# Optimization experiments

Hardware: AMD Instinct MI355X
Metric: run time of the kernel (lower is better)

## Reference

```python
import jax, jax.numpy as jnp
import numpy as np

B, N, K = 16, 2048, 20
EPS = 1e-5
NEG_SLOPE = 0.01


def gsa(x, k):
    # graph_self_attention. x: (B, D, N)
    xx = jnp.sum(x * x, axis=1)                              # (B, N)
    inner = jnp.einsum('bdn,bdm->bnm', x, x)                 # (B, N, N)
    dist = 2.0 * inner - xx[:, :, None] - xx[:, None, :]
    s, idx = jax.lax.top_k(dist, k)                          # (B, N, k) nearest (incl. self)
    xt = jnp.transpose(x, (0, 2, 1))                         # (B, N, D)
    nn_feat = jax.vmap(lambda f, i: f[i])(xt, idx)           # (B, N, k, D) irregular gather
    diff = nn_feat - xt[:, :, None, :]                       # neighbor - center
    w = jax.nn.softmax(s, axis=-1)                           # (B, N, k)
    agg = jnp.einsum('bnk,bnkd->bnd', w, diff)               # (B, N, D)
    return jnp.transpose(jnp.concatenate([xt, agg], axis=2), (0, 2, 1))  # (B, 2D, N)


def conv_bn_lrelu(x, W, gamma, beta):
    # 1x1 Conv1d (no bias) + BatchNorm1d (training-mode batch stats) + LeakyReLU(0.01)
    y = jnp.einsum('oc,bcn->bon', W, x)
    mean = jnp.mean(y, axis=(0, 2), keepdims=True)
    var = jnp.var(y, axis=(0, 2), keepdims=True)
    y = (y - mean) * jax.lax.rsqrt(var + EPS)
    y = gamma[None, :, None] * y + beta[None, :, None]
    return jnp.where(y >= 0, y, NEG_SLOPE * y)


def setup_inputs() -> dict:
    key = jax.random.key(0)
    ks = jax.random.split(key, 6)
    x = jax.random.normal(ks[0], (B, 3, N), jnp.float32)

    def w(kk, o, c):
        return jax.random.normal(kk, (o, c), jnp.float32) * (1.0 / np.sqrt(c).astype(np.float32))

    inp = {
        'x': x,
        'W1': w(ks[1], 64, 6),
        'W2': w(ks[2], 64, 128),
        'W3': w(ks[3], 128, 128),
        'W4': w(ks[4], 256, 256),
        'W5': w(ks[5], 512, 512),
    }
    for i, c in zip(range(1, 6), (64, 64, 128, 256, 512)):
        inp[f'g{i}'] = jnp.ones((c,), jnp.float32)
        inp[f'b{i}'] = jnp.zeros((c,), jnp.float32)
    return inp


def reference(x, W1, W2, W3, W4, W5, g1, b1, g2, b2, g3, b3, g4, b4, g5, b5):
    k = K
    x1 = conv_bn_lrelu(gsa(x, k), W1, g1, b1)     # (B, 64, N)
    x2 = conv_bn_lrelu(gsa(x1, k), W2, g2, b2)    # (B, 64, N)
    x3 = conv_bn_lrelu(gsa(x2, k), W3, g3, b3)    # (B, 128, N)
    x4 = conv_bn_lrelu(gsa(x3, k), W4, g4, b4)    # (B, 256, N)
    cat = jnp.concatenate([x1, x2, x3, x4], axis=1)  # (B, 512, N)
    x5 = conv_bn_lrelu(cat, W5, g5, b5)              # (B, 512, N)
    return (x5, x3)
```

## Files before the change

kernel.cpp:

```cpp
#include <hip/hip_runtime.h>
#include <math.h>

#define B_ 16
#define N_ 2048
#define KNN 20
#define BN_EPS 1e-5f
#define SLOPE 0.01f

__global__ __launch_bounds__(256) void xx_kernel(const float* __restrict__ xin, long bstr, int D,
                                                 float* __restrict__ xx) {
  int i = blockIdx.x * 256 + threadIdx.x;
  if (i >= B_ * N_) return;
  int b = i >> 11, n = i & (N_ - 1);
  const float* p = xin + (long)b * bstr + n;
  float s = 0.f;
#pragma unroll 1
  for (int d = 0; d < D; ++d) { float v = p[(long)d * N_]; s = fmaf(v, v, s); }
  xx[i] = s;
}

__global__ __launch_bounds__(256) void transpose_kernel(const float* __restrict__ xin, long bstr,
                                                        float* __restrict__ xT, long xTbstr, int D) {
  __shared__ float s[32][65];
  int b = blockIdx.y;
  int n0 = blockIdx.x * 64;
  int tid = threadIdx.x;
  const float* xb = xin + (long)b * bstr;
  float* tb = xT + (long)b * xTbstr;
  for (int dc = 0; dc < D; dc += 32) {
    for (int i = tid; i < 32 * 64; i += 256) {
      int d = i >> 6, n = i & 63;
      s[d][n] = (dc + d < D) ? xb[(long)(dc + d) * N_ + n0 + n] : 0.f;
    }
    __syncthreads();
    for (int i = tid; i < 64 * 32; i += 256) {
      int n = i >> 5, d = i & 31;
      if (dc + d < D) tb[(long)(n0 + n) * D + dc + d] = s[d][n];
    }
    __syncthreads();
  }
}

template <int D>
__global__ __launch_bounds__(256, 2) void gsa_stream_kernel(const float* __restrict__ xin, long bstr,
                                                            const float* __restrict__ xT, long xTbstr,
                                                            const float* __restrict__ xx,
                                                            float* __restrict__ agg, long aggbstr) {
  constexpr int NV = (D + 63) / 64;
  __shared__ float xn_s[16][((D + 3) & ~3)];
  int tid = threadIdx.x, w = tid >> 6, lane = tid & 63;
  int r0 = blockIdx.x * 16;
  int b = r0 >> 11, n0 = r0 & (N_ - 1);
  const float* xb = xin + (long)b * bstr;
  const float* tb = xT + (long)b * xTbstr;
  for (int i = tid; i < 16 * D; i += 256) {
    int rr = i / D, d = i - rr * D;
    xn_s[rr][d] = tb[(long)(n0 + rr) * D + d];
  }
  __syncthreads();

  float4 acc[4][8];
#pragma unroll
  for (int r = 0; r < 4; ++r)
#pragma unroll
    for (int c = 0; c < 8; ++c) acc[r][c] = make_float4(0.f, 0.f, 0.f, 0.f);

  float4 bufA[8], bufB[8];
  {
    const float4* xrow = (const float4*)xb;
#pragma unroll
    for (int c = 0; c < 8; ++c) bufA[c] = xrow[c * 64 + lane];
  }

#define FMA_STEP(BUF, dd)                                              \
  {                                                                    \
    _Pragma("unroll") for (int r = 0; r < 4; ++r) {                    \
      float xnd = xn_s[(w << 2) + r][dd];                              \
      _Pragma("unroll") for (int c = 0; c < 8; ++c) {                  \
        acc[r][c].x = fmaf(xnd, BUF[c].x, acc[r][c].x);                \
        acc[r][c].y = fmaf(xnd, BUF[c].y, acc[r][c].y);                \
        acc[r][c].z = fmaf(xnd, BUF[c].z, acc[r][c].z);                \
        acc[r][c].w = fmaf(xnd, BUF[c].w, acc[r][c].w);                \
      }                                                                \
    }                                                                  \
  }

#pragma unroll 1
  for (int d = 0; d < D; d += 2) {
    if (d + 1 < D) {
      const float4* xrow = (const float4*)(xb + (long)(d + 1) * N_);
#pragma unroll
      for (int c = 0; c < 8; ++c) bufB[c] = xrow[c * 64 + lane];
    }
    FMA_STEP(bufA, d);
    if (d + 2 < D) {
      const float4* xrow = (const float4*)(xb + (long)(d + 2) * N_);
#pragma unroll
      for (int c = 0; c < 8; ++c) bufA[c] = xrow[c * 64 + lane];
    }
    if (d + 1 < D) FMA_STEP(bufB, d + 1);
  }
#undef FMA_STEP

  {
    const float4* xx4 = (const float4*)(xx + (long)b * N_);
    float4 xm[8];
#pragma unroll
    for (int c = 0; c < 8; ++c) xm[c] = xx4[c * 64 + lane];
#pragma unroll
    for (int r = 0; r < 4; ++r) {
      float xxn = xx[(long)b * N_ + n0 + (w << 2) + r];
#pragma unroll
      for (int c = 0; c < 8; ++c) {
        acc[r][c].x = 2.f * acc[r][c].x - xxn - xm[c].x;
        acc[r][c].y = 2.f * acc[r][c].y - xxn - xm[c].y;
        acc[r][c].z = 2.f * acc[r][c].z - xxn - xm[c].z;
        acc[r][c].w = 2.f * acc[r][c].w - xxn - xm[c].w;
      }
    }
  }

  float m8[4][8];
  int sspack[4];
#pragma unroll
  for (int r = 0; r < 4; ++r) {
    int sp = 0;
#pragma unroll
    for (int c = 0; c < 8; ++c) {
      const float* av = (const float*)&acc[r][c];
      float mm = av[0]; int ss = 0;
      if (av[1] > mm) { mm = av[1]; ss = 1; }
      if (av[2] > mm) { mm = av[2]; ss = 2; }
      if (av[3] > mm) { mm = av[3]; ss = 3; }
      m8[r][c] = mm; sp |= ss << (2 * c);
    }
    sspack[r] = sp;
  }

  float Z[4] = {0.f, 0.f, 0.f, 0.f};
  float m0[4];
  float ve[4][NV];
#pragma unroll
  for (int r = 0; r < 4; ++r)
#pragma unroll
    for (int vi = 0; vi < NV; ++vi) ve[r][vi] = 0.f;

#pragma unroll 1
  for (int it = 0; it < KNN; ++it) {
    float best[4]; int bidx[4];
#pragma unroll
    for (int r = 0; r < 4; ++r) {
      int sp = sspack[r];
      float bv = m8[r][0]; int bi = (lane << 2) + (sp & 3);
#pragma unroll
      for (int c = 1; c < 8; ++c) {
        float v = m8[r][c];
        int cand = (c << 8) + (lane << 2) + ((sp >> (2 * c)) & 3);
        if (v > bv) { bv = v; bi = cand; }
      }
      best[r] = bv; bidx[r] = bi;
    }
#pragma unroll
    for (int off = 1; off < 64; off <<= 1) {
#pragma unroll
      for (int r = 0; r < 4; ++r) {
        float ov = __shfl_xor(best[r], off);
        int oi = __shfl_xor(bidx[r], off);
        if (ov > best[r] || (ov == best[r] && oi < bidx[r])) { best[r] = ov; bidx[r] = oi; }
      }
    }
#pragma unroll
    for (int r = 0; r < 4; ++r) {
      int ub = __builtin_amdgcn_readfirstlane(bidx[r]);
      if (it == 0) m0[r] = best[r];
      float e = __expf(best[r] - m0[r]);
      Z[r] += e;
#pragma unroll
      for (int vi = 0; vi < NV; ++vi) {
        int dd = lane + (vi << 6);
        if (D >= 64 || dd < D) ve[r][vi] = fmaf(e, tb[(long)ub * D + dd], ve[r][vi]);
      }
      int cw = ub >> 8, jw = ub & 3;
      bool isw = (lane == ((ub >> 2) & 63));
#pragma unroll
      for (int c = 0; c < 8; ++c)
        if (c == cw) {
          float* av = (float*)&acc[r][c];
#pragma unroll
          for (int j = 0; j < 4; ++j)
            if (j == jw && isw) av[j] = -3.4e38f;
          float mm = av[0]; int ss = 0;
          if (av[1] > mm) { mm = av[1]; ss = 1; }
          if (av[2] > mm) { mm = av[2]; ss = 2; }
          if (av[3] > mm) { mm = av[3]; ss = 3; }
          m8[r][c] = mm;
          sspack[r] = (sspack[r] & ~(3 << (2 * c))) | (ss << (2 * c));
        }
    }
  }

#pragma unroll
  for (int r = 0; r < 4; ++r) {
    float rZ = 1.f / Z[r];
    int n = n0 + (w << 2) + r;
#pragma unroll
    for (int vi = 0; vi < NV; ++vi) {
      int dd = lane + (vi << 6);
      if (D >= 64 || dd < D)
        agg[(long)b * aggbstr + (long)dd * N_ + n] = ve[r][vi] * rZ - xn_s[(w << 2) + r][dd];
    }
  }
}

__global__ __launch_bounds__(256) void gemm_bn_kernel(const float* __restrict__ Wm, int O, int K,
                                                      const float* __restrict__ xin, long bstr, int Dx,
                                                      const float* __restrict__ agg, long aggbstr,
                                                      float* __restrict__ y, float* __restrict__ stats) {
  __shared__ __align__(16) float As[16][68];
  __shared__ __align__(16) float Bs[16][68];
  int tid = threadIdx.x;
  int o0 = blockIdx.x * 64;
  int j0 = blockIdx.y * 64;
  int b = j0 >> 11, n0 = j0 & (N_ - 1);
  int ty = tid >> 4, tx = tid & 15;
  float accr[4][4] = {};
  int aK = tid & 15, aO = tid >> 4;
  int bK = tid >> 4, bn4 = (tid & 15) << 2;
  for (int k0 = 0; k0 < K; k0 += 16) {
#pragma unroll
    for (int q = 0; q < 4; ++q) {
      int o = aO + (q << 4);
      As[aK][o] = (k0 + aK < K) ? Wm[(long)(o0 + o) * K + k0 + aK] : 0.f;
    }
    {
      int c = k0 + bK;
      float4 v = {0.f, 0.f, 0.f, 0.f};
      if (c < K) {
        const float* src = (c < Dx) ? xin + (long)b * bstr + (long)c * N_
                                    : agg + (long)b * aggbstr + (long)(c - Dx) * N_;
        v = *(const float4*)(src + n0 + bn4);
      }
      *(float4*)&Bs[bK][bn4] = v;
    }
    __syncthreads();
#pragma unroll
    for (int kk = 0; kk < 16; ++kk) {
      float4 a4 = *(const float4*)&As[kk][ty << 2];
      float4 b4 = *(const float4*)&Bs[kk][tx << 2];
      accr[0][0] = fmaf(a4.x, b4.x, accr[0][0]);
      accr[0][1] = fmaf(a4.x, b4.y, accr[0][1]);
      accr[0][2] = fmaf(a4.x, b4.z, accr[0][2]);
      accr[0][3] = fmaf(a4.x, b4.w, accr[0][3]);
      accr[1][0] = fmaf(a4.y, b4.x, accr[1][0]);
      accr[1][1] = fmaf(a4.y, b4.y, accr[1][1]);
      accr[1][2] = fmaf(a4.y, b4.z, accr[1][2]);
      accr[1][3] = fmaf(a4.y, b4.w, accr[1][3]);
      accr[2][0] = fmaf(a4.z, b4.x, accr[2][0]);
      accr[2][1] = fmaf(a4.z, b4.y, accr[2][1]);
      accr[2][2] = fmaf(a4.z, b4.z, accr[2][2]);
      accr[2][3] = fmaf(a4.z, b4.w, accr[2][3]);
      accr[3][0] = fmaf(a4.w, b4.x, accr[3][0]);
      accr[3][1] = fmaf(a4.w, b4.y, accr[3][1]);
      accr[3][2] = fmaf(a4.w, b4.z, accr[3][2]);
      accr[3][3] = fmaf(a4.w, b4.w, accr[3][3]);
    }
    __syncthreads();
  }
#pragma unroll
  for (int r = 0; r < 4; ++r) {
    int o = o0 + (ty << 2) + r;
    float4 v;
    v.x = accr[r][0]; v.y = accr[r][1]; v.z = accr[r][2]; v.w = accr[r][3];
    *(float4*)(y + ((long)b * O + o) * N_ + n0 + bn4) = v;
    float s1 = v.x + v.y + v.z + v.w;
    float s2 = v.x * v.x + v.y * v.y + v.z * v.z + v.w * v.w;
#pragma unroll
    for (int off = 1; off < 16; off <<= 1) { s1 += __shfl_xor(s1, off); s2 += __shfl_xor(s2, off); }
    if (tx == 0) { atomicAdd(&stats[o], s1); atomicAdd(&stats[O + o], s2); }
  }
}

__global__ __launch_bounds__(256) void gemm_bn128_kernel(const float* __restrict__ Wm, int O, int K,
                                                         const float* __restrict__ xin, long bstr, int Dx,
                                                         const float* __restrict__ agg, long aggbstr,
                                                         float* __restrict__ y, float* __restrict__ stats) {
  __shared__ __align__(16) float As[8][132];
  __shared__ __align__(16) float Bs[8][132];
  int tid = threadIdx.x;
  int o0 = blockIdx.x * 128;
  int j0 = blockIdx.y * 128;
  int b = j0 >> 11, n0 = j0 & (N_ - 1);
  int ty = tid >> 4, tx = tid & 15;
  float acc[8][8] = {};
  int aO = tid & 127, aKb = tid >> 7;
  int bK = tid >> 5, bj4 = (tid & 31) << 2;
#pragma unroll 1
  for (int k0 = 0; k0 < K; k0 += 8) {
    __syncthreads();
#pragma unroll
    for (int q = 0; q < 4; ++q) {
      int kk = aKb + (q << 1);
      As[kk][aO] = Wm[(long)(o0 + aO) * K + k0 + kk];
    }
    {
      int c = k0 + bK;
      const float* src = (c < Dx) ? xin + (long)b * bstr + (long)c * N_
                                  : agg + (long)b * aggbstr + (long)(c - Dx) * N_;
      *(float4*)&Bs[bK][bj4] = *(const float4*)(src + n0 + bj4);
    }
    __syncthreads();
#pragma unroll
    for (int kk = 0; kk < 8; ++kk) {
      float4 alo = *(const float4*)&As[kk][ty << 2];
      float4 ahi = *(const float4*)&As[kk][64 + (ty << 2)];
      float4 blo = *(const float4*)&Bs[kk][tx << 2];
      float4 bhi = *(const float4*)&Bs[kk][64 + (tx << 2)];
      float av[8] = {alo.x, alo.y, alo.z, alo.w, ahi.x, ahi.y, ahi.z, ahi.w};
      float bv[8] = {blo.x, blo.y, blo.z, blo.w, bhi.x, bhi.y, bhi.z, bhi.w};
#pragma unroll
      for (int r = 0; r < 8; ++r)
#pragma unroll
        for (int c = 0; c < 8; ++c) acc[r][c] = fmaf(av[r], bv[c], acc[r][c]);
    }
  }
#pragma unroll
  for (int r = 0; r < 8; ++r) {
    int o = o0 + ((r < 4) ? (ty << 2) + r : 64 + (ty << 2) + (r - 4));
    float4 vlo, vhi;
    vlo.x = acc[r][0]; vlo.y = acc[r][1]; vlo.z = acc[r][2]; vlo.w = acc[r][3];
    vhi.x = acc[r][4]; vhi.y = acc[r][5]; vhi.z = acc[r][6]; vhi.w = acc[r][7];
    float* yrow = y + ((long)b * O + o) * N_ + n0;
    *(float4*)(yrow + (tx << 2)) = vlo;
    *(float4*)(yrow + 64 + (tx << 2)) = vhi;
    float s1 = vlo.x + vlo.y + vlo.z + vlo.w + vhi.x + vhi.y + vhi.z + vhi.w;
    float s2 = vlo.x * vlo.x + vlo.y * vlo.y + vlo.z * vlo.z + vlo.w * vlo.w +
               vhi.x * vhi.x + vhi.y * vhi.y + vhi.z * vhi.z + vhi.w * vhi.w;
#pragma unroll
    for (int off = 1; off < 16; off <<= 1) { s1 += __shfl_xor(s1, off); s2 += __shfl_xor(s2, off); }
    if (tx == 0) { atomicAdd(&stats[o], s1); atomicAdd(&stats[O + o], s2); }
  }
}

__global__ __launch_bounds__(256) void bn_finalize_kernel(float* __restrict__ stats,
                                                          const float* __restrict__ g,
                                                          const float* __restrict__ be, int O) {
  int o = blockIdx.x * 256 + threadIdx.x;
  if (o >= O) return;
  const float inv_cnt = 1.f / (B_ * (float)N_);
  float mean = stats[o] * inv_cnt;
  float var = stats[O + o] * inv_cnt - mean * mean;
  float a = g[o] * rsqrtf(var + BN_EPS);
  float bb = be[o] - mean * a;
  stats[o] = a;
  stats[O + o] = bb;
}

__global__ __launch_bounds__(256) void bn_apply_kernel(const float* __restrict__ y,
                                                       const float* __restrict__ stats, int O,
                                                       float* __restrict__ dst, int c0, int dstStride,
                                                       float* __restrict__ dst2) {
  long i4 = (long)blockIdx.x * 256 + threadIdx.x;
  long total4 = (long)B_ * O * N_ / 4;
  if (i4 >= total4) return;
  long i = i4 << 2;
  int ob = __ffs(O) - 1;
  int o = (int)((i >> 11) & (O - 1));
  int b = (int)(i >> (11 + ob));
  int n = (int)(i & (N_ - 1));
  float a = stats[o], bb = stats[O + o];
  float4 v = *(const float4*)(y + i);
  v.x = fmaf(a, v.x, bb); v.x = v.x >= 0.f ? v.x : SLOPE * v.x;
  v.y = fmaf(a, v.y, bb); v.y = v.y >= 0.f ? v.y : SLOPE * v.y;
  v.z = fmaf(a, v.z, bb); v.z = v.z >= 0.f ? v.z : SLOPE * v.z;
  v.w = fmaf(a, v.w, bb); v.w = v.w >= 0.f ? v.w : SLOPE * v.w;
  *(float4*)(dst + ((long)b * dstStride + c0 + o) * N_ + n) = v;
  if (dst2) *(float4*)(dst2 + i) = v;
}

extern "C" void kernel_launch(void* const* d_in, const int* in_sizes, int n_in,
                              void* d_out, int out_size, void* d_ws, size_t ws_size,
                              hipStream_t stream) {
  const float* x = (const float*)d_in[0];
  const float* W[5];
  const float* gm[5];
  const float* bt[5];
  for (int i = 0; i < 5; ++i) W[i] = (const float*)d_in[1 + i];
  for (int i = 0; i < 5; ++i) { gm[i] = (const float*)d_in[6 + 2 * i]; bt[i] = (const float*)d_in[7 + 2 * i]; }

  const long XBS = 512L * N_;
  float* xall = (float*)d_ws;
  float* xxb = xall + (long)B_ * XBS;
  float* stats = xxb + (long)B_ * N_;
  float* xTb = xall + 256L * N_;
  float* aggb = xall + 384L * N_;
  float* yb = (float*)d_out;
  float* outB = (float*)d_out + (long)B_ * XBS;

  hipMemsetAsync(stats, 0, 5 * 1024 * sizeof(float), stream);

  struct LayerCfg { const float* xin; long bstr; int D; int O; int c0; };
  LayerCfg L[4] = {
      {x, 3L * N_, 3, 64, 0},
      {xall, XBS, 64, 64, 64},
      {xall + 64L * N_, XBS, 64, 128, 128},
      {xall + 128L * N_, XBS, 128, 256, 256},
  };

  for (int li = 0; li < 4; ++li) {
    const LayerCfg c = L[li];
    float* st = stats + li * 1024;
    xx_kernel<<<B_ * N_ / 256, 256, 0, stream>>>(c.xin, c.bstr, c.D, xxb);
    transpose_kernel<<<dim3(N_ / 64, B_), 256, 0, stream>>>(c.xin, c.bstr, xTb, XBS, c.D);
    if (c.D == 3)
      gsa_stream_kernel<3><<<B_ * N_ / 16, 256, 0, stream>>>(c.xin, c.bstr, xTb, XBS, xxb, aggb, XBS);
    else if (c.D == 64)
      gsa_stream_kernel<64><<<B_ * N_ / 16, 256, 0, stream>>>(c.xin, c.bstr, xTb, XBS, xxb, aggb, XBS);
    else
      gsa_stream_kernel<128><<<B_ * N_ / 16, 256, 0, stream>>>(c.xin, c.bstr, xTb, XBS, xxb, aggb, XBS);
    int K = 2 * c.D;
    if (c.O >= 128 && (K % 8) == 0)
      gemm_bn128_kernel<<<dim3(c.O / 128, B_ * N_ / 128), 256, 0, stream>>>(
          W[li], c.O, K, c.xin, c.bstr, c.D, aggb, XBS, yb, st);
    else
      gemm_bn_kernel<<<dim3(c.O / 64, B_ * N_ / 64), 256, 0, stream>>>(
          W[li], c.O, K, c.xin, c.bstr, c.D, aggb, XBS, yb, st);
    bn_finalize_kernel<<<(c.O + 255) / 256, 256, 0, stream>>>(st, gm[li], bt[li], c.O);
    long t4 = (long)B_ * c.O * N_ / 4;
    bn_apply_kernel<<<(int)((t4 + 255) / 256), 256, 0, stream>>>(
        yb, st, c.O, xall, c.c0, 512, (li == 2) ? outB : nullptr);
  }
  {
    float* st = stats + 4 * 1024;
    gemm_bn128_kernel<<<dim3(512 / 128, B_ * N_ / 128), 256, 0, stream>>>(
        W[4], 512, 512, xall, XBS, 512, nullptr, XBS, yb, st);
    bn_finalize_kernel<<<2, 256, 0, stream>>>(st, gm[4], bt[4], 512);
    long t4 = (long)B_ * 512 * N_ / 4;
    bn_apply_kernel<<<(int)((t4 + 255) / 256), 256, 0, stream>>>(yb, st, 512, yb, 0, 512, nullptr);
  }
}
```

Measured before the change: 2.285 ms.

## Compute kNN distance matrix with split-fp16 MFMA instead of scalar FP32 FMAs

Replaces the scalar FP32 outer-product distance loop with MFMA 16x16x32 f16 instructions. Each feature is split into high and low fp16 halves and three MFMAs per tile give roughly FP32 accuracy. The transpose kernel now writes padded hi/lo fp16 planes, and each wave owns a 512-column slice. Top-k selection is restructured to reduce across the four waves through shared memory with two barriers per iteration. Neighbor gathers read the fp16 pairs. The cost is tie and rounding risk in kNN selection, plus extra synchronization in the selection loop.

Result: slower. 4.633 ms (+102.7%).

```diff
diff --git a/kernel.cpp b/kernel.cpp
--- a/kernel.cpp
+++ b/kernel.cpp
@@ -6,6 +6,10 @@
 #define KNN 20
 #define BN_EPS 1e-5f
 #define SLOPE 0.01f
+
+typedef float f32x4 __attribute__((ext_vector_type(4)));
+typedef _Float16 f16x8 __attribute__((ext_vector_type(8)));
+typedef unsigned short ushort_t;
 
 __global__ __launch_bounds__(256) void xx_kernel(const float* __restrict__ xin, long bstr, int D,
                                                  float* __restrict__ xx) {
@@ -19,15 +23,17 @@
   xx[i] = s;
 }
 
-__global__ __launch_bounds__(256) void transpose_kernel(const float* __restrict__ xin, long bstr,
-                                                        float* __restrict__ xT, long xTbstr, int D) {
+__global__ __launch_bounds__(256) void split_kernel(const float* __restrict__ xin, long bstr,
+                                                    int D, int DP,
+                                                    ushort_t* __restrict__ xT, long xTbstr_us) {
   __shared__ float s[32][65];
   int b = blockIdx.y;
   int n0 = blockIdx.x * 64;
   int tid = threadIdx.x;
   const float* xb = xin + (long)b * bstr;
-  float* tb = xT + (long)b * xTbstr;
-  for (int dc = 0; dc < D; dc += 32) {
+  ushort_t* xh = xT + (long)b * xTbstr_us;
+  ushort_t* xl = xh + 2048 * DP;
+  for (int dc = 0; dc < DP; dc += 32) {
     for (int i = tid; i < 32 * 64; i += 256) {
       int d = i >> 6, n = i & 63;
       s[d][n] = (dc + d < D) ? xb[(long)(dc + d) * N_ + n0 + n] : 0.f;
@@ -35,168 +41,170 @@
     __syncthreads();
     for (int i = tid; i < 64 * 32; i += 256) {
       int n = i >> 5, d = i & 31;
-      if (dc + d < D) tb[(long)(n0 + n) * D + dc + d] = s[d][n];
-    }
-    __syncthreads();
-  }
-}
-
-template <int D>
-__global__ __launch_bounds__(256, 2) void gsa_stream_kernel(const float* __restrict__ xin, long bstr,
-                                                            const float* __restrict__ xT, long xTbstr,
-                                                            const float* __restrict__ xx,
-                                                            float* __restrict__ agg, long aggbstr) {
-  constexpr int NV = (D + 63) / 64;
-  __shared__ float xn_s[16][((D + 3) & ~3)];
+      float v = s[d][n];
+      _Float16 h = (_Float16)v;
+      float r1 = v - (float)h;
+      _Float16 l = (_Float16)r1;
+      long idx = (long)(n0 + n) * DP + dc + d;
+      *(_Float16*)&xh[idx] = h;
+      *(_Float16*)&xl[idx] = l;
+    }
+    __syncthreads();
+  }
+}
+
+template <int D, int DP, int NV>
+__global__ __launch_bounds__(256) void gsa_tour_kernel(const ushort_t* __restrict__ xT,
+                                                       long xTbstr_us,
+                                                       const float* __restrict__ xx,
+                                                       float* __restrict__ agg, long aggbstr) {
+  __shared__ float red_v[4][16];
+  __shared__ int red_c[4][16];
   int tid = threadIdx.x, w = tid >> 6, lane = tid & 63;
+  int lo16 = lane & 15, hi4 = lane >> 4;
   int r0 = blockIdx.x * 16;
   int b = r0 >> 11, n0 = r0 & (N_ - 1);
-  const float* xb = xin + (long)b * bstr;
-  const float* tb = xT + (long)b * xTbstr;
-  for (int i = tid; i < 16 * D; i += 256) {
-    int rr = i / D, d = i - rr * D;
-    xn_s[rr][d] = tb[(long)(n0 + rr) * D + d];
-  }
-  __syncthreads();
-
-  float4 acc[4][8];
-#pragma unroll
-  for (int r = 0; r < 4; ++r)
-#pragma unroll
-    for (int c = 0; c < 8; ++c) acc[r][c] = make_float4(0.f, 0.f, 0.f, 0.f);
-
-  float4 bufA[8], bufB[8];
-  {
-    const float4* xrow = (const float4*)xb;
-#pragma unroll
-    for (int c = 0; c < 8; ++c) bufA[c] = xrow[c * 64 + lane];
-  }
-
-#define FMA_STEP(BUF, dd)                                              \
-  {                                                                    \
-    _Pragma("unroll") for (int r = 0; r < 4; ++r) {                    \
-      float xnd = xn_s[(w << 2) + r][dd];                              \
-      _Pragma("unroll") for (int c = 0; c < 8; ++c) {                  \
-        acc[r][c].x = fmaf(xnd, BUF[c].x, acc[r][c].x);                \
-        acc[r][c].y = fmaf(xnd, BUF[c].y, acc[r][c].y);                \
-        acc[r][c].z = fmaf(xnd, BUF[c].z, acc[r][c].z);                \
-        acc[r][c].w = fmaf(xnd, BUF[c].w, acc[r][c].w);                \
-      }                                                                \
-    }                                                                  \
-  }
+  const ushort_t* xTb = xT + (long)b * xTbstr_us;
+  int wcol0 = w << 9;
+
+  f32x4 acc[32];
+#pragma unroll
+  for (int t = 0; t < 32; ++t) acc[t] = (f32x4){0.f, 0.f, 0.f, 0.f};
 
 #pragma unroll 1
-  for (int d = 0; d < D; d += 2) {
-    if (d + 1 < D) {
-      const float4* xrow = (const float4*)(xb + (long)(d + 1) * N_);
-#pragma unroll
-      for (int c = 0; c < 8; ++c) bufB[c] = xrow[c * 64 + lane];
-    }
-    FMA_STEP(bufA, d);
-    if (d + 2 < D) {
-      const float4* xrow = (const float4*)(xb + (long)(d + 2) * N_);
-#pragma unroll
-      for (int c = 0; c < 8; ++c) bufA[c] = xrow[c * 64 + lane];
-    }
-    if (d + 1 < D) FMA_STEP(bufB, d + 1);
-  }
-#undef FMA_STEP
-
-  {
-    const float4* xx4 = (const float4*)(xx + (long)b * N_);
-    float4 xm[8];
-#pragma unroll
-    for (int c = 0; c < 8; ++c) xm[c] = xx4[c * 64 + lane];
-#pragma unroll
-    for (int r = 0; r < 4; ++r) {
-      float xxn = xx[(long)b * N_ + n0 + (w << 2) + r];
-#pragma unroll
-      for (int c = 0; c < 8; ++c) {
-        acc[r][c].x = 2.f * acc[r][c].x - xxn - xm[c].x;
-        acc[r][c].y = 2.f * acc[r][c].y - xxn - xm[c].y;
-        acc[r][c].z = 2.f * acc[r][c].z - xxn - xm[c].z;
-        acc[r][c].w = 2.f * acc[r][c].w - xxn - xm[c].w;
-      }
-    }
+  for (int ks = 0; ks < DP / 32; ++ks) {
+    const ushort_t* ab = xTb + (long)(n0 + lo16) * DP + ks * 32 + hi4 * 8;
+    f16x8 ah = *(const f16x8*)ab;
+    f16x8 al = *(const f16x8*)(ab + 2048 * DP);
+#pragma unroll
+    for (int t = 0; t < 32; ++t) {
+      const ushort_t* bb = xTb + (long)(wcol0 + t * 16 + lo16) * DP + ks * 32 + hi4 * 8;
+      f16x8 bh = *(const f16x8*)bb;
+      f16x8 bl = *(const f16x8*)(bb + 2048 * DP);
+      acc[t] = __builtin_amdgcn_mfma_f32_16x16x32_f16(ah, bh, acc[t], 0, 0, 0);
+      acc[t] = __builtin_amdgcn_mfma_f32_16x16x32_f16(ah, bl, acc[t], 0, 0, 0);
+      acc[t] = __builtin_amdgcn_mfma_f32_16x16x32_f16(al, bh, acc[t], 0, 0, 0);
+    }
+  }
+
+  float xxr[4];
+#pragma unroll
+  for (int q = 0; q < 4; ++q) xxr[q] = xx[b * N_ + n0 + hi4 * 4 + q];
+#pragma unroll
+  for (int t = 0; t < 32; ++t) {
+    float xxc = xx[b * N_ + wcol0 + t * 16 + lo16];
+#pragma unroll
+    for (int q = 0; q < 4; ++q) acc[t][q] = 2.f * acc[t][q] - xxr[q] - xxc;
   }
 
   float m8[4][8];
   int sspack[4];
 #pragma unroll
-  for (int r = 0; r < 4; ++r) {
+  for (int q = 0; q < 4; ++q) {
     int sp = 0;
 #pragma unroll
     for (int c = 0; c < 8; ++c) {
-      const float* av = (const float*)&acc[r][c];
-      float mm = av[0]; int ss = 0;
-      if (av[1] > mm) { mm = av[1]; ss = 1; }
-      if (av[2] > mm) { mm = av[2]; ss = 2; }
-      if (av[3] > mm) { mm = av[3]; ss = 3; }
-      m8[r][c] = mm; sp |= ss << (2 * c);
-    }
-    sspack[r] = sp;
+      float mm = acc[4 * c][q]; int ss = 0;
+      if (acc[4 * c + 1][q] > mm) { mm = acc[4 * c + 1][q]; ss = 1; }
+      if (acc[4 * c + 2][q] > mm) { mm = acc[4 * c + 2][q]; ss = 2; }
+      if (acc[4 * c + 3][q] > mm) { mm = acc[4 * c + 3][q]; ss = 3; }
+      m8[q][c] = mm; sp |= ss << (2 * c);
+    }
+    sspack[q] = sp;
   }
 
   float Z[4] = {0.f, 0.f, 0.f, 0.f};
-  float m0[4];
+  float m0[4] = {0.f, 0.f, 0.f, 0.f};
   float ve[4][NV];
 #pragma unroll
   for (int r = 0; r < 4; ++r)
 #pragma unroll
     for (int vi = 0; vi < NV; ++vi) ve[r][vi] = 0.f;
 
+  int wc_base = wcol0 + lo16;
 #pragma unroll 1
   for (int it = 0; it < KNN; ++it) {
-    float best[4]; int bidx[4];
+    float bv[4]; int bc[4];
+#pragma unroll
+    for (int q = 0; q < 4; ++q) {
+      int sp = sspack[q];
+      float bvq = m8[q][0]; int bcq = wc_base + ((sp & 3) << 4);
+#pragma unroll
+      for (int c = 1; c < 8; ++c) {
+        float v = m8[q][c];
+        int cc = wc_base + (c << 6) + (((sp >> (2 * c)) & 3) << 4);
+        if (v > bvq) { bvq = v; bcq = cc; }
+      }
+      bv[q] = bvq; bc[q] = bcq;
+    }
+#pragma unroll
+    for (int off = 1; off < 16; off <<= 1) {
+#pragma unroll
+      for (int q = 0; q < 4; ++q) {
+        float ov = __shfl_xor(bv[q], off);
+        int oc = __shfl_xor(bc[q], off);
+        if (ov > bv[q] || (ov == bv[q] && oc < bc[q])) { bv[q] = ov; bc[q] = oc; }
+      }
+    }
+    if (lo16 == 0) {
+#pragma unroll
+      for (int q = 0; q < 4; ++q) {
+        red_v[w][hi4 * 4 + q] = bv[q];
+        red_c[w][hi4 * 4 + q] = bc[q];
+      }
+    }
+    __syncthreads();
+#pragma unroll
+    for (int q = 0; q < 4; ++q) {
+      int row = hi4 * 4 + q;
+      float gv = red_v[0][row]; int gc = red_c[0][row];
+#pragma unroll
+      for (int j = 1; j < 4; ++j) {
+        float vj = red_v[j][row]; int cj = red_c[j][row];
+        if (vj > gv || (vj == gv && cj < gc)) { gv = vj; gc = cj; }
+      }
+      if ((gc >> 9) == w) {
+        int rel = gc - wcol0;
+        int cw = rel >> 6, jw = (rel >> 4) & 3;
+        bool amw = (lo16 == (rel & 15));
+#pragma unroll
+        for (int c = 0; c < 8; ++c)
+          if (c == cw) {
+#pragma unroll
+            for (int j = 0; j < 4; ++j)
+              if (j == jw && amw) acc[4 * c + j][q] = -3.4e38f;
+            float mm = acc[4 * c][q]; int ss = 0;
+            if (acc[4 * c + 1][q] > mm) { mm = acc[4 * c + 1][q]; ss = 1; }
+            if (acc[4 * c + 2][q] > mm) { mm = acc[4 * c + 2][q]; ss = 2; }
+            if (acc[4 * c + 3][q] > mm) { mm = acc[4 * c + 3][q]; ss = 3; }
+            m8[q][c] = mm;
+            sspack[q] = (sspack[q] & ~(3 << (2 * c))) | (ss << (2 * c));
+          }
+      }
+    }
 #pragma unroll
     for (int r = 0; r < 4; ++r) {
-      int sp = sspack[r];
-      float bv = m8[r][0]; int bi = (lane << 2) + (sp & 3);
-#pragma unroll
-      for (int c = 1; c < 8; ++c) {
-        float v = m8[r][c];
-        int cand = (c << 8) + (lane << 2) + ((sp >> (2 * c)) & 3);
-        if (v > bv) { bv = v; bi = cand; }
-      }
-      best[r] = bv; bidx[r] = bi;
-    }
-#pragma unroll
-    for (int off = 1; off < 64; off <<= 1) {
-#pragma unroll
-      for (int r = 0; r < 4; ++r) {
-        float ov = __shfl_xor(best[r], off);
-        int oi = __shfl_xor(bidx[r], off);
-        if (ov > best[r] || (ov == best[r] && oi < bidx[r])) { best[r] = ov; bidx[r] = oi; }
-      }
-    }
-#pragma unroll
-    for (int r = 0; r < 4; ++r) {
-      int ub = __builtin_amdgcn_readfirstlane(bidx[r]);
-      if (it == 0) m0[r] = best[r];
-      float e = __expf(best[r] - m0[r]);
+      int row = (w << 2) + r;
+      float gv = red_v[0][row]; int gc = red_c[0][row];
+#pragma unroll
+      for (int j = 1; j < 4; ++j) {
+        float vj = red_v[j][row]; int cj = red_c[j][row];
+        if (vj > gv || (vj == gv && cj < gc)) { gv = vj; gc = cj; }
+      }
+      if (it == 0) m0[r] = gv;
+      float e = __expf(gv - m0[r]);
       Z[r] += e;
 #pragma unroll
       for (int vi = 0; vi < NV; ++vi) {
         int dd = lane + (vi << 6);
-        if (D >= 64 || dd < D) ve[r][vi] = fmaf(e, tb[(long)ub * D + dd], ve[r][vi]);
-      }
-      int cw = ub >> 8, jw = ub & 3;
-      bool isw = (lane == ((ub >> 2) & 63));
-#pragma unroll
-      for (int c = 0; c < 8; ++c)
-        if (c == cw) {
-          float* av = (float*)&acc[r][c];
-#pragma unroll
-          for (int j = 0; j < 4; ++j)
-            if (j == jw && isw) av[j] = -3.4e38f;
-          float mm = av[0]; int ss = 0;
-          if (av[1] > mm) { mm = av[1]; ss = 1; }
-          if (av[2] > mm) { mm = av[2]; ss = 2; }
-          if (av[3] > mm) { mm = av[3]; ss = 3; }
-          m8[r][c] = mm;
-          sspack[r] = (sspack[r] & ~(3 << (2 * c))) | (ss << (2 * c));
+        if (D >= 64 || dd < D) {
+          const ushort_t* pp = xTb + (long)gc * DP + dd;
+          float xv = (float)(*(const _Float16*)pp) + (float)(*(const _Float16*)(pp + 2048 * DP));
+          ve[r][vi] = fmaf(e, xv, ve[r][vi]);
         }
-    }
+      }
+    }
+    __syncthreads();
   }
 
 #pragma unroll
@@ -206,8 +214,11 @@
 #pragma unroll
     for (int vi = 0; vi < NV; ++vi) {
       int dd = lane + (vi << 6);
-      if (D >= 64 || dd < D)
-        agg[(long)b * aggbstr + (long)dd * N_ + n] = ve[r][vi] * rZ - xn_s[(w << 2) + r][dd];
+      if (D >= 64 || dd < D) {
+        const ushort_t* pn = xTb + (long)n * DP + dd;
+        float xn = (float)(*(const _Float16*)pn) + (float)(*(const _Float16*)(pn + 2048 * DP));
+        agg[(long)b * aggbstr + (long)dd * N_ + n] = ve[r][vi] * rZ - xn;
+      }
     }
   }
 }
@@ -391,32 +402,33 @@
   float* xall = (float*)d_ws;
   float* xxb = xall + (long)B_ * XBS;
   float* stats = xxb + (long)B_ * N_;
-  float* xTb = xall + 256L * N_;
+  ushort_t* xTbase = (ushort_t*)(xall + 256L * N_);
+  const long xTbstr_us = XBS * 2;
   float* aggb = xall + 384L * N_;
   float* yb = (float*)d_out;
   float* outB = (float*)d_out + (long)B_ * XBS;
 
   hipMemsetAsync(stats, 0, 5 * 1024 * sizeof(float), stream);
 
-  struct LayerCfg { const float* xin; long bstr; int D; int O; int c0; };
+  struct LayerCfg { const float* xin; long bstr; int D; int DP; int O; int c0; };
   LayerCfg L[4] = {
-      {x, 3L * N_, 3, 64, 0},
-      {xall, XBS, 64, 64, 64},
-      {xall + 64L * N_, XBS, 64, 128, 128},
-      {xall + 128L * N_, XBS, 128, 256, 256},
+      {x, 3L * N_, 3, 32, 64, 0},
+      {xall, XBS, 64, 64, 64, 64},
+      {xall + 64L * N_, XBS, 64, 64, 128, 128},
+      {xall + 128L * N_, XBS, 128, 128, 256, 256},
   };
 
   for (int li = 0; li < 4; ++li) {
     const LayerCfg c = L[li];
     float* st = stats + li * 1024;
     xx_kernel<<<B_ * N_ / 256, 256, 0, stream>>>(c.xin, c.bstr, c.D, xxb);
-    transpose_kernel<<<dim3(N_ / 64, B_), 256, 0, stream>>>(c.xin, c.bstr, xTb, XBS, c.D);
+    split_kernel<<<dim3(N_ / 64, B_), 256, 0, stream>>>(c.xin, c.bstr, c.D, c.DP, xTbase, xTbstr_us);
     if (c.D == 3)
-      gsa_stream_kernel<3><<<B_ * N_ / 16, 256, 0, stream>>>(c.xin, c.bstr, xTb, XBS, xxb, aggb, XBS);
+      gsa_tour_kernel<3, 32, 1><<<B_ * N_ / 16, 256, 0, stream>>>(xTbase, xTbstr_us, xxb, aggb, XBS);
     else if (c.D == 64)
-      gsa_stream_kernel<64><<<B_ * N_ / 16, 256, 0, stream>>>(c.xin, c.bstr, xTb, XBS, xxb, aggb, XBS);
+      gsa_tour_kernel<64, 64, 1><<<B_ * N_ / 16, 256, 0, stream>>>(xTbase, xTbstr_us, xxb, aggb, XBS);
     else
-      gsa_stream_kernel<128><<<B_ * N_ / 16, 256, 0, stream>>>(c.xin, c.bstr, xTb, XBS, xxb, aggb, XBS);
+      gsa_tour_kernel<128, 128, 2><<<B_ * N_ / 16, 256, 0, stream>>>(xTbase, xTbstr_us, xxb, aggb, XBS);
     int K = 2 * c.D;
     if (c.O >= 128 && (K % 8) == 0)
       gemm_bn128_kernel<<<dim3(c.O / 128, B_ * N_ / 128), 256, 0, stream>>>(
```
